# Optimization experiments

Measured on AMD Instinct MI355X. Metric: run time of the kernel, lower is better.

The kernel has to match this reference:

```python
import jax, jax.numpy as jnp
import numpy as np

V = 50000   # words_num
D = 128     # embedding_dim
B = 2048    # batch
P = 20      # max Huffman path length


def setup_inputs() -> dict:
    key = jax.random.key(0)
    k1, k2, k3, k4, k5 = jax.random.split(key, 5)
    inputs_vector = jax.random.uniform(k1, (B, V), dtype=jnp.float32)
    path_nodes_indices = jax.random.randint(k2, (B, P), 0, V)
    huffman_codes = jax.random.randint(k3, (B, P), 0, 2).astype(jnp.float32)
    mask = jnp.ones((B, P), dtype=jnp.float32)
    # learned params, torch nn.Linear weight layout [out, in], kaiming-uniform-ish scale
    W_emb = jax.random.uniform(k4, (D, V), dtype=jnp.float32, minval=-1.0, maxval=1.0) / np.sqrt(V)
    W_cls = jax.random.uniform(k5, (V, D), dtype=jnp.float32, minval=-1.0, maxval=1.0) / np.sqrt(D)
    return {
        "inputs_vector": inputs_vector,
        "W_emb": W_emb,
        "W_cls": W_cls,
        "path_nodes_indices": path_nodes_indices,
        "huffman_codes": huffman_codes,
        "mask": mask,
    }


def _bce_with_logits(logits, targets):
    # numerically stable, elementwise (reduction='none')
    return jnp.maximum(logits, 0.0) - logits * targets + jnp.log1p(jnp.exp(-jnp.abs(logits)))


def reference(inputs_vector, W_emb, W_cls, path_nodes_indices, huffman_codes, mask):
    x = inputs_vector @ W_emb.T              # [B, D]  embedding Linear (no bias)
    logits_full = x @ W_cls.T                # [B, V]  full-vocab cls matmul (as in source)
    logits = jnp.take_along_axis(logits_full, path_nodes_indices, axis=1)  # [B, P]
    loss = _bce_with_logits(logits, huffman_codes)  # [B, P]
    masked_loss = loss * mask
    per_sample = masked_loss.sum(axis=-1) / mask.sum(axis=-1)  # [B]
    return per_sample.mean()
```

## Files before the change

kernel.cpp:

```cpp
#include <hip/hip_runtime.h>
#include <hip/hip_bf16.h>

#define V 50000
#define D 128
#define B 2048
#define P 20

#define BM 128
#define NSPLIT 32
#define KC 1568
#define VPAD (NSPLIT * KC)
#define NSLICE (VPAD / 32)
#define NMT (B / BM)

typedef float  f32x4  __attribute__((ext_vector_type(4)));
typedef short  bf16x8 __attribute__((ext_vector_type(8)));
typedef unsigned int uint4v __attribute__((ext_vector_type(4)));

__device__ __forceinline__ unsigned int pk2(float a, float b) {
    return (__float_as_uint(b) & 0xFFFF0000u) | (__float_as_uint(a) >> 16);
}
__device__ __forceinline__ unsigned short f2bf(float f) {
    unsigned int u = __float_as_uint(f);
    return (unsigned short)((u + 0x7FFFu + ((u >> 16) & 1u)) >> 16);
}
__device__ __forceinline__ bf16x8 pack8(f32x4 lo, f32x4 hi) {
    union { uint4v u; bf16x8 h; } r;
    r.u.x = pk2(lo[0], lo[1]); r.u.y = pk2(lo[2], lo[3]);
    r.u.z = pk2(hi[0], hi[1]); r.u.w = pk2(hi[2], hi[3]);
    return r.h;
}
__device__ __forceinline__ void gload_lds16(const void* g, void* l) {
    __builtin_amdgcn_global_load_lds(
        (const __attribute__((address_space(1))) unsigned int*)g,
        (__attribute__((address_space(3))) unsigned int*)l, 16, 0, 0);
}

__global__ __launch_bounds__(256)
void w2v_wcast(const float* __restrict__ Wemb, unsigned short* __restrict__ WTF) {
    __shared__ unsigned short L[128 * 128];
    const int bk = blockIdx.x;
    const int t  = threadIdx.x;
    const int d = t >> 1, h = t & 1;
    const float* src = Wemb + (size_t)d * V + bk * 128 + h * 64;
#pragma unroll
    for (int j = 0; j < 8; ++j) {
        const int kg = bk * 128 + h * 64 + j * 8;
        f32x4 v0 = {0,0,0,0}, v1 = {0,0,0,0};
        if (kg + 8 <= V) {
            const f32x4* p = reinterpret_cast<const f32x4*>(src + j * 8);
            v0 = p[0]; v1 = p[1];
        }
        uint4v u;
        u.x = pk2(v0[0], v0[1]); u.y = pk2(v0[2], v0[3]);
        u.z = pk2(v1[0], v1[1]); u.w = pk2(v1[2], v1[3]);
        const int c8 = h * 8 + j;
        *reinterpret_cast<uint4v*>((char*)L + d * 256 + ((c8 ^ (d & 15)) << 4)) = u;
    }
    __syncthreads();
    const int w = t >> 6, l = t & 63;
    const int kg4 = l >> 4, fr = l & 15;
#pragma unroll
    for (int sl = 0; sl < 4; ++sl)
#pragma unroll
        for (int j2 = 0; j2 < 2; ++j2) {
            const int n  = w + j2 * 4;
            const int dd = n * 16 + fr;
            const int c8 = sl * 4 + kg4;
            uint4v u = *reinterpret_cast<const uint4v*>(
                (char*)L + dd * 256 + ((c8 ^ (dd & 15)) << 4));
            *reinterpret_cast<uint4v*>(
                (char*)WTF + ((size_t)(bk * 4 + sl) * 8 + n) * 1024 + l * 16) = u;
        }
}

template<int FAST>
__global__ __launch_bounds__(256, 2)
void w2v_gemm(const float* __restrict__ Ain, const void* __restrict__ Wsrc,
              void* __restrict__ part) {
    __shared__ char smem[65536];
    char* Wlds = smem + 32768;

    const int i   = blockIdx.x;
    const int xcd = i & 7;
    const int q   = i >> 3;
    const int s   = xcd * 4 + (q >> 4);
    const int mt  = q & 15;
    const int m0  = mt * BM;
    const int k0  = s * KC;
    const int kend = (k0 + KC < V) ? (k0 + KC) : V;
    const int nst  = (kend - k0 + 63) >> 6;

    const int tid  = threadIdx.x;
    const int lane = tid & 63;
    const int wid  = tid >> 6;
    const int w32  = wid * 32;
    const int fr   = lane & 15;
    const int kg4  = lane >> 4;

    f32x4 acc[2][8] = {};

    const int arow = tid >> 1;
    const int ah   = tid & 1;
    const float* aSrc = Ain + (size_t)(m0 + arow) * V + ah * 32;
    const unsigned short* WT = (const unsigned short*)Wsrc;
    const float*          Wf = (const float*)Wsrc;

    f32x4 aR[8];
    auto loadA = [&](int ks) {
#pragma unroll
        for (int j = 0; j < 8; ++j) {
            const bool ok = (ks + ah * 32 + j * 4 + 4 <= kend);
            const f32x4* p = reinterpret_cast<const f32x4*>(ok ? (aSrc + ks + j * 4)
                                                               : (aSrc + k0));
            f32x4 v = *p;
            if (!ok) v = f32x4{0.f, 0.f, 0.f, 0.f};
            aR[j] = v;
        }
    };
    auto writeA = [&](int buf) {
        char* base = smem + buf * 16384 + arow * 128;
#pragma unroll
        for (int j2 = 0; j2 < 4; ++j2) {
            uint4v u;
            u.x = pk2(aR[j2*2][0], aR[j2*2][1]);   u.y = pk2(aR[j2*2][2], aR[j2*2][3]);
            u.z = pk2(aR[j2*2+1][0], aR[j2*2+1][1]); u.w = pk2(aR[j2*2+1][2], aR[j2*2+1][3]);
            const int c8 = ah * 4 + j2;
            *reinterpret_cast<uint4v*>(base + ((c8 ^ (arow & 7)) << 4)) = u;
        }
    };
    auto stageW = [&](int buf, int ks5) {
#pragma unroll
        for (int j = 0; j < 4; ++j) {
            const int g = wid * 4 + j;
            const unsigned short* gp = WT + (size_t)(ks5 + (g >> 3)) * 4096
                                          + (g & 7) * 512 + lane * 8;
            gload_lds16(gp, Wlds + buf * 16384 + g * 1024);
        }
    };
    auto computeMicro = [&](int buf, int u) {
        bf16x8 af[2];
#pragma unroll
        for (int m = 0; m < 2; ++m) {
            const int r  = w32 + m * 16 + fr;
            const int c8 = u * 4 + kg4;
            af[m] = *reinterpret_cast<const bf16x8*>(
                smem + buf * 16384 + r * 128 + ((c8 ^ (r & 7)) << 4));
        }
#pragma unroll
        for (int n = 0; n < 8; ++n) {
            const bf16x8 wf = *reinterpret_cast<const bf16x8*>(
                Wlds + buf * 16384 + (u * 8 + n) * 1024 + lane * 16);
            acc[0][n] = __builtin_amdgcn_mfma_f32_16x16x32_bf16(af[0], wf, acc[0][n], 0, 0, 0);
            acc[1][n] = __builtin_amdgcn_mfma_f32_16x16x32_bf16(af[1], wf, acc[1][n], 0, 0, 0);
        }
    };

    if (FAST) {
        loadA(k0);
        stageW(0, s * 49);
        for (int t = 0; t < nst; ++t) {
            writeA(t & 1);
            const bool more = (t + 1 < nst);
            if (more) {
                loadA(k0 + (t + 1) * 64);
                stageW((t + 1) & 1, s * 49 + (t + 1) * 2);
                asm volatile("s_waitcnt vmcnt(12) lgkmcnt(0)" ::: "memory");
            } else {
                asm volatile("s_waitcnt vmcnt(0) lgkmcnt(0)" ::: "memory");
            }
            __builtin_amdgcn_s_barrier();
            computeMicro(t & 1, 0);
            computeMicro(t & 1, 1);
        }
    } else {
        bf16x8 wfr[8];
        for (int t = 0; t < nst; ++t) {
            const int ks = k0 + t * 64;
            loadA(ks);
            writeA(0);
            __syncthreads();
#pragma unroll
            for (int u = 0; u < 2; ++u) {
#pragma unroll
                for (int n = 0; n < 8; ++n) {
                    const int kg = ks + u * 32 + kg4 * 8;
                    f32x4 lo = {0,0,0,0}, hi = {0,0,0,0};
                    if (kg + 8 <= V) {
                        const f32x4* p = reinterpret_cast<const f32x4*>(
                            Wf + (size_t)(n * 16 + fr) * V + kg);
                        lo = p[0]; hi = p[1];
                    }
                    wfr[n] = pack8(lo, hi);
                }
                bf16x8 af[2];
#pragma unroll
                for (int m = 0; m < 2; ++m) {
                    const int r  = w32 + m * 16 + fr;
                    const int c8 = u * 4 + kg4;
                    af[m] = *reinterpret_cast<const bf16x8*>(
                        smem + r * 128 + ((c8 ^ (r & 7)) << 4));
                }
#pragma unroll
                for (int n = 0; n < 8; ++n) {
                    acc[0][n] = __builtin_amdgcn_mfma_f32_16x16x32_bf16(af[0], wfr[n], acc[0][n], 0, 0, 0);
                    acc[1][n] = __builtin_amdgcn_mfma_f32_16x16x32_bf16(af[1], wfr[n], acc[1][n], 0, 0, 0);
                }
            }
            __syncthreads();
        }
    }

    if (!FAST) {
        float* outp = (float*)part;
#pragma unroll
        for (int m = 0; m < 2; ++m) {
            const int r0 = m0 + w32 + m * 16 + kg4 * 4;
#pragma unroll
            for (int n = 0; n < 8; ++n) {
                const int c = n * 16 + fr;
#pragma unroll
                for (int jj = 0; jj < 4; ++jj)
                    atomicAdd(&outp[(size_t)(r0 + jj) * D + c], acc[m][n][jj]);
            }
        }
        return;
    }
    asm volatile("s_waitcnt lgkmcnt(0)" ::: "memory");
    __builtin_amdgcn_s_barrier();
    unsigned short* Cs = (unsigned short*)smem;
#pragma unroll
    for (int m = 0; m < 2; ++m) {
        const int r0 = w32 + m * 16 + kg4 * 4;
#pragma unroll
        for (int n = 0; n < 8; ++n) {
            const int c = n * 16 + fr;
#pragma unroll
            for (int jj = 0; jj < 4; ++jj)
                Cs[(r0 + jj) * 128 + c] = f2bf(acc[m][n][jj]);
        }
    }
    __syncthreads();
    char* dstb = (char*)part + ((size_t)s * B + m0) * (D * 2);
#pragma unroll
    for (int it = 0; it < 8; ++it) {
        const int off = (it * 256 + tid) * 16;
        uint4v v = *reinterpret_cast<const uint4v*>((char*)smem + off);
        *reinterpret_cast<uint4v*>(dstb + off) = v;
    }
}

__global__ __launch_bounds__(256)
void w2v_loss(const void* __restrict__ part, int part_bf16,
              const float* __restrict__ Wcls, const int* __restrict__ pathIdx,
              const float* __restrict__ codes, const float* __restrict__ mask,
              float* __restrict__ out) {
    const int lane = threadIdx.x & 63;
    const int wid  = threadIdx.x >> 6;
    const int b    = blockIdx.x * 4 + wid;

    float x0 = 0.f, x1 = 0.f;
    if (part_bf16) {
        const unsigned* pb = (const unsigned*)part;
#pragma unroll 8
        for (int s = 0; s < NSPLIT; ++s) {
            unsigned u = pb[((size_t)s * B + b) * 64 + lane];
            x0 += __uint_as_float(u << 16);
            x1 += __uint_as_float(u & 0xFFFF0000u);
        }
    } else {
        const float* pf = (const float*)part;
        const float2 v = *reinterpret_cast<const float2*>(&pf[(size_t)b * D + lane * 2]);
        x0 = v.x; x1 = v.y;
    }

    float lsum = 0.f, msum = 0.f;
#pragma unroll
    for (int p = 0; p < P; ++p) {
        int node = pathIdx[b * P + p];
        const float2 w = *reinterpret_cast<const float2*>(&Wcls[(size_t)node * D + lane * 2]);
        float d = x0 * w.x + x1 * w.y;
#pragma unroll
        for (int off = 1; off < 64; off <<= 1)
            d += __shfl_xor(d, off, 64);
        float t  = codes[b * P + p];
        float mm = mask[b * P + p];
        float loss = fmaxf(d, 0.f) - d * t + log1pf(__expf(-fabsf(d)));
        lsum += loss * mm;
        msum += mm;
    }
    float per = (msum > 0.f) ? (lsum / msum) : 0.f;

    __shared__ float wsum[4];
    if (lane == 0) wsum[wid] = per;
    __syncthreads();
    if (threadIdx.x == 0) {
        float ssum = wsum[0] + wsum[1] + wsum[2] + wsum[3];
        atomicAdd(out, ssum * (1.0f / (float)B));
    }
}

extern "C" void kernel_launch(void* const* d_in, const int* in_sizes, int n_in,
                              void* d_out, int out_size, void* d_ws, size_t ws_size,
                              hipStream_t stream) {
    const float* inputs = (const float*)d_in[0];
    const float* W_emb  = (const float*)d_in[1];
    const float* W_cls  = (const float*)d_in[2];
    const int*   path   = (const int*)  d_in[3];
    const float* codes  = (const float*)d_in[4];
    const float* mask   = (const float*)d_in[5];
    float* out = (float*)d_out;

    hipMemsetAsync(d_out, 0, sizeof(float), stream);

    const size_t wtf_bytes = (size_t)NSLICE * 8192;
    const size_t part_off  = (wtf_bytes + 255) & ~(size_t)255;
    const size_t part_need = part_off + (size_t)NSPLIT * B * D * 2;

    if (ws_size >= part_need) {
        unsigned short* WTF = (unsigned short*)d_ws;
        char* partp = (char*)d_ws + part_off;
        w2v_wcast<<<dim3(VPAD / 128), dim3(256), 0, stream>>>(W_emb, WTF);
        w2v_gemm<1><<<dim3(NMT * NSPLIT), dim3(256), 0, stream>>>(inputs, WTF, partp);
        w2v_loss<<<dim3(B / 4), dim3(256), 0, stream>>>(partp, 1, W_cls, path, codes, mask, out);
    } else {
        hipMemsetAsync(d_ws, 0, (size_t)B * D * sizeof(float), stream);
        w2v_gemm<0><<<dim3(NMT * NSPLIT), dim3(256), 0, stream>>>(inputs, W_emb, d_ws);
        w2v_loss<<<dim3(B / 4), dim3(256), 0, stream>>>(d_ws, 0, W_cls, path, codes, mask, out);
    }
}
```

Before: 170.6 us.

## Stage whole A K-chunk in LDS upfront and stream W from registers

Restructures the split-K GEMM: tiles shrink to 64 rows with 896-wide K chunks over 56 splits and 512-thread blocks. Each block loads its entire A slice into LDS once, converting to bf16 before a single barrier. W fragments are then read straight from global memory into double-buffered registers, replacing the per-step LDS staging and barriers. This is meant to remove per-iteration synchronisation and expose more parallelism, at the cost of larger LDS per block, more partial sums for the loss kernel to reduce, and no overlap between the A load and compute.

```diff
diff --git a/kernel.cpp b/kernel.cpp
--- a/kernel.cpp
+++ b/kernel.cpp
@@ -6,9 +6,10 @@
 #define B 2048
 #define P 20
 
-#define BM 128
-#define NSPLIT 32
-#define KC 1568
+#define BM 64
+#define KC 896
+#define NSTEP 14
+#define NSPLIT 56
 #define VPAD (NSPLIT * KC)
 #define NSLICE (VPAD / 32)
 #define NMT (B / BM)
@@ -16,6 +17,7 @@
 typedef float  f32x4  __attribute__((ext_vector_type(4)));
 typedef short  bf16x8 __attribute__((ext_vector_type(8)));
 typedef unsigned int uint4v __attribute__((ext_vector_type(4)));
+typedef unsigned int uint2v __attribute__((ext_vector_type(2)));
 
 __device__ __forceinline__ unsigned int pk2(float a, float b) {
     return (__float_as_uint(b) & 0xFFFF0000u) | (__float_as_uint(a) >> 16);
@@ -29,11 +31,6 @@
     r.u.x = pk2(lo[0], lo[1]); r.u.y = pk2(lo[2], lo[3]);
     r.u.z = pk2(hi[0], hi[1]); r.u.w = pk2(hi[2], hi[3]);
     return r.h;
-}
-__device__ __forceinline__ void gload_lds16(const void* g, void* l) {
-    __builtin_amdgcn_global_load_lds(
-        (const __attribute__((address_space(1))) unsigned int*)g,
-        (__attribute__((address_space(3))) unsigned int*)l, 16, 0, 0);
 }
 
 __global__ __launch_bounds__(256)
@@ -75,178 +72,125 @@
 }
 
 template<int FAST>
-__global__ __launch_bounds__(256, 2)
+__global__ __launch_bounds__(512, 2)
 void w2v_gemm(const float* __restrict__ Ain, const void* __restrict__ Wsrc,
               void* __restrict__ part) {
-    __shared__ char smem[65536];
-    char* Wlds = smem + 32768;
+    __shared__ char smem[NSTEP * 8192];
 
     const int i   = blockIdx.x;
     const int xcd = i & 7;
-    const int q   = i >> 3;
-    const int s   = xcd * 4 + (q >> 4);
-    const int mt  = q & 15;
+    const int j   = i >> 3;
+    const int s   = xcd * 7 + (j >> 5);
+    const int mt  = j & 31;
     const int m0  = mt * BM;
     const int k0  = s * KC;
     const int kend = (k0 + KC < V) ? (k0 + KC) : V;
-    const int nst  = (kend - k0 + 63) >> 6;
 
     const int tid  = threadIdx.x;
     const int lane = tid & 63;
     const int wid  = tid >> 6;
-    const int w32  = wid * 32;
+    const int rg   = wid & 3;
+    const int wc   = wid >> 2;
     const int fr   = lane & 15;
     const int kg4  = lane >> 4;
 
-    f32x4 acc[2][8] = {};
-
-    const int arow = tid >> 1;
-    const int ah   = tid & 1;
-    const float* aSrc = Ain + (size_t)(m0 + arow) * V + ah * 32;
+    {
+        const int row = tid >> 3;
+        const int q   = tid & 7;
+        const float* src = Ain + (size_t)(m0 + row) * V + k0 + q * 112;
+        char* wbase = smem + row * 128;
+#pragma unroll
+        for (int jj = 0; jj < 28; ++jj) {
+            const int f0 = q * 112 + jj * 4;
+            f32x4 v = {0.f, 0.f, 0.f, 0.f};
+            if (k0 + f0 + 4 <= kend)
+                v = *reinterpret_cast<const f32x4*>(src + jj * 4);
+            uint2v u; u.x = pk2(v[0], v[1]); u.y = pk2(v[2], v[3]);
+            const int tt = f0 >> 6, c8 = (f0 >> 3) & 7, hf = (f0 >> 2) & 1;
+            *reinterpret_cast<uint2v*>(wbase + tt * 8192 + ((c8 ^ (row & 7)) << 4) + hf * 8) = u;
+        }
+    }
+    __syncthreads();
+
+    f32x4 acc[4] = {};
     const unsigned short* WT = (const unsigned short*)Wsrc;
     const float*          Wf = (const float*)Wsrc;
 
-    f32x4 aR[8];
-    auto loadA = [&](int ks) {
-#pragma unroll
-        for (int j = 0; j < 8; ++j) {
-            const bool ok = (ks + ah * 32 + j * 4 + 4 <= kend);
-            const f32x4* p = reinterpret_cast<const f32x4*>(ok ? (aSrc + ks + j * 4)
-                                                               : (aSrc + k0));
-            f32x4 v = *p;
-            if (!ok) v = f32x4{0.f, 0.f, 0.f, 0.f};
-            aR[j] = v;
-        }
-    };
-    auto writeA = [&](int buf) {
-        char* base = smem + buf * 16384 + arow * 128;
-#pragma unroll
-        for (int j2 = 0; j2 < 4; ++j2) {
-            uint4v u;
-            u.x = pk2(aR[j2*2][0], aR[j2*2][1]);   u.y = pk2(aR[j2*2][2], aR[j2*2][3]);
-            u.z = pk2(aR[j2*2+1][0], aR[j2*2+1][1]); u.w = pk2(aR[j2*2+1][2], aR[j2*2+1][3]);
-            const int c8 = ah * 4 + j2;
-            *reinterpret_cast<uint4v*>(base + ((c8 ^ (arow & 7)) << 4)) = u;
-        }
-    };
-    auto stageW = [&](int buf, int ks5) {
-#pragma unroll
-        for (int j = 0; j < 4; ++j) {
-            const int g = wid * 4 + j;
-            const unsigned short* gp = WT + (size_t)(ks5 + (g >> 3)) * 4096
-                                          + (g & 7) * 512 + lane * 8;
-            gload_lds16(gp, Wlds + buf * 16384 + g * 1024);
-        }
-    };
-    auto computeMicro = [&](int buf, int u) {
-        bf16x8 af[2];
-#pragma unroll
-        for (int m = 0; m < 2; ++m) {
-            const int r  = w32 + m * 16 + fr;
-            const int c8 = u * 4 + kg4;
-            af[m] = *reinterpret_cast<const bf16x8*>(
-                smem + buf * 16384 + r * 128 + ((c8 ^ (r & 7)) << 4));
-        }
-#pragma unroll
-        for (int n = 0; n < 8; ++n) {
-            const bf16x8 wf = *reinterpret_cast<const bf16x8*>(
-                Wlds + buf * 16384 + (u * 8 + n) * 1024 + lane * 16);
-            acc[0][n] = __builtin_amdgcn_mfma_f32_16x16x32_bf16(af[0], wf, acc[0][n], 0, 0, 0);
-            acc[1][n] = __builtin_amdgcn_mfma_f32_16x16x32_bf16(af[1], wf, acc[1][n], 0, 0, 0);
-        }
-    };
-
-    if (FAST) {
-        loadA(k0);
-        stageW(0, s * 49);
-        for (int t = 0; t < nst; ++t) {
-            writeA(t & 1);
-            const bool more = (t + 1 < nst);
-            if (more) {
-                loadA(k0 + (t + 1) * 64);
-                stageW((t + 1) & 1, s * 49 + (t + 1) * 2);
-                asm volatile("s_waitcnt vmcnt(12) lgkmcnt(0)" ::: "memory");
-            } else {
-                asm volatile("s_waitcnt vmcnt(0) lgkmcnt(0)" ::: "memory");
-            }
-            __builtin_amdgcn_s_barrier();
-            computeMicro(t & 1, 0);
-            computeMicro(t & 1, 1);
-        }
-    } else {
-        bf16x8 wfr[8];
-        for (int t = 0; t < nst; ++t) {
-            const int ks = k0 + t * 64;
-            loadA(ks);
-            writeA(0);
-            __syncthreads();
-#pragma unroll
-            for (int u = 0; u < 2; ++u) {
-#pragma unroll
-                for (int n = 0; n < 8; ++n) {
-                    const int kg = ks + u * 32 + kg4 * 8;
+    bf16x8 wfA[8], wfB[8];
+    auto loadW = [&](bf16x8* wf, int t) {
+        if (FAST) {
+            const size_t ks5 = (size_t)s * 28 + t * 2;
+#pragma unroll
+            for (int u = 0; u < 2; ++u)
+#pragma unroll
+                for (int n = 0; n < 4; ++n)
+                    wf[u * 4 + n] = *reinterpret_cast<const bf16x8*>(
+                        (const char*)WT + (ks5 + u) * 8192 + (wc * 4 + n) * 1024 + lane * 16);
+        } else {
+#pragma unroll
+            for (int u = 0; u < 2; ++u)
+#pragma unroll
+                for (int n = 0; n < 4; ++n) {
+                    const int kg = k0 + t * 64 + u * 32 + kg4 * 8;
+                    const int dd = wc * 64 + n * 16 + fr;
                     f32x4 lo = {0,0,0,0}, hi = {0,0,0,0};
                     if (kg + 8 <= V) {
-                        const f32x4* p = reinterpret_cast<const f32x4*>(
-                            Wf + (size_t)(n * 16 + fr) * V + kg);
+                        const f32x4* p = reinterpret_cast<const f32x4*>(Wf + (size_t)dd * V + kg);
                         lo = p[0]; hi = p[1];
                     }
-                    wfr[n] = pack8(lo, hi);
+                    wf[u * 4 + n] = pack8(lo, hi);
                 }
-                bf16x8 af[2];
-#pragma unroll
-                for (int m = 0; m < 2; ++m) {
-                    const int r  = w32 + m * 16 + fr;
-                    const int c8 = u * 4 + kg4;
-                    af[m] = *reinterpret_cast<const bf16x8*>(
-                        smem + r * 128 + ((c8 ^ (r & 7)) << 4));
-                }
-#pragma unroll
-                for (int n = 0; n < 8; ++n) {
-                    acc[0][n] = __builtin_amdgcn_mfma_f32_16x16x32_bf16(af[0], wfr[n], acc[0][n], 0, 0, 0);
-                    acc[1][n] = __builtin_amdgcn_mfma_f32_16x16x32_bf16(af[1], wfr[n], acc[1][n], 0, 0, 0);
-                }
-            }
-            __syncthreads();
-        }
-    }
+        }
+    };
+    auto computeStep = [&](const bf16x8* wf, int t) {
+#pragma unroll
+        for (int u = 0; u < 2; ++u) {
+            const int r = rg * 16 + fr;
+            const bf16x8 af = *reinterpret_cast<const bf16x8*>(
+                smem + t * 8192 + r * 128 + (((u * 4 + kg4) ^ (r & 7)) << 4));
+#pragma unroll
+            for (int n = 0; n < 4; ++n)
+                acc[n] = __builtin_amdgcn_mfma_f32_16x16x32_bf16(af, wf[u * 4 + n], acc[n], 0, 0, 0);
+        }
+    };
+
+    loadW(wfA, 0);
+#pragma unroll
+    for (int t = 0; t < NSTEP; t += 2) {
+        loadW(wfB, t + 1);
+        computeStep(wfA, t);
+        if (t + 2 < NSTEP) loadW(wfA, t + 2);
+        computeStep(wfB, t + 1);
+    }
+
+    __syncthreads();
 
     if (!FAST) {
         float* outp = (float*)part;
 #pragma unroll
-        for (int m = 0; m < 2; ++m) {
-            const int r0 = m0 + w32 + m * 16 + kg4 * 4;
-#pragma unroll
-            for (int n = 0; n < 8; ++n) {
-                const int c = n * 16 + fr;
-#pragma unroll
-                for (int jj = 0; jj < 4; ++jj)
-                    atomicAdd(&outp[(size_t)(r0 + jj) * D + c], acc[m][n][jj]);
-            }
+        for (int n = 0; n < 4; ++n) {
+            const int c = wc * 64 + n * 16 + fr;
+#pragma unroll
+            for (int jj = 0; jj < 4; ++jj)
+                atomicAdd(&outp[(size_t)(m0 + rg * 16 + kg4 * 4 + jj) * D + c], acc[n][jj]);
         }
         return;
     }
-    asm volatile("s_waitcnt lgkmcnt(0)" ::: "memory");
-    __builtin_amdgcn_s_barrier();
     unsigned short* Cs = (unsigned short*)smem;
 #pragma unroll
-    for (int m = 0; m < 2; ++m) {
-        const int r0 = w32 + m * 16 + kg4 * 4;
-#pragma unroll
-        for (int n = 0; n < 8; ++n) {
-            const int c = n * 16 + fr;
-#pragma unroll
-            for (int jj = 0; jj < 4; ++jj)
-                Cs[(r0 + jj) * 128 + c] = f2bf(acc[m][n][jj]);
-        }
+    for (int n = 0; n < 4; ++n) {
+        const int c = wc * 64 + n * 16 + fr;
+#pragma unroll
+        for (int jj = 0; jj < 4; ++jj)
+            Cs[(rg * 16 + kg4 * 4 + jj) * 128 + c] = f2bf(acc[n][jj]);
     }
     __syncthreads();
     char* dstb = (char*)part + ((size_t)s * B + m0) * (D * 2);
 #pragma unroll
-    for (int it = 0; it < 8; ++it) {
-        const int off = (it * 256 + tid) * 16;
-        uint4v v = *reinterpret_cast<const uint4v*>((char*)smem + off);
-        *reinterpret_cast<uint4v*>(dstb + off) = v;
+    for (int it = 0; it < 2; ++it) {
+        const int off = (it * 512 + tid) * 16;
+        *reinterpret_cast<uint4v*>(dstb + off) =
+            *reinterpret_cast<const uint4v*>(smem + off);
     }
 }
 
@@ -321,11 +265,11 @@
         unsigned short* WTF = (unsigned short*)d_ws;
         char* partp = (char*)d_ws + part_off;
         w2v_wcast<<<dim3(VPAD / 128), dim3(256), 0, stream>>>(W_emb, WTF);
-        w2v_gemm<1><<<dim3(NMT * NSPLIT), dim3(256), 0, stream>>>(inputs, WTF, partp);
+        w2v_gemm<1><<<dim3(NMT * NSPLIT), dim3(512), 0, stream>>>(inputs, WTF, partp);
         w2v_loss<<<dim3(B / 4), dim3(256), 0, stream>>>(partp, 1, W_cls, path, codes, mask, out);
     } else {
         hipMemsetAsync(d_ws, 0, (size_t)B * D * sizeof(float), stream);
-        w2v_gemm<0><<<dim3(NMT * NSPLIT), dim3(256), 0, stream>>>(inputs, W_emb, d_ws);
+        w2v_gemm<0><<<dim3(NMT * NSPLIT), dim3(512), 0, stream>>>(inputs, W_emb, d_ws);
         w2v_loss<<<dim3(B / 4), dim3(256), 0, stream>>>(d_ws, 0, W_cls, path, codes, mask, out);
     }
 }
```

Result: slower. 248.1 us (+45.5%).

## Make A tiles wave-private in LDS, load W fragments directly to registers

Applied to the files above, without the earlier changes.

Each wave now stages only its own 32 rows of the A tile into a private LDS region laid out in MFMA fragment order. This removes the block-wide barrier from the K loop. W fragments are read straight from global memory into registers instead of through global_load_lds staging, which halves LDS use and allows 3 blocks per CU. The K split also goes from 32 to 48 chunks to fill more CUs. The trade-offs are that each wave re-reads W from global/L2 with less latency hiding, and there are more partial outputs to reduce. The epilogue also dropped its pre-barrier, which may be unsafe now that Cs overlays other waves' LDS regions.

```diff
diff --git a/kernel.cpp b/kernel.cpp
--- a/kernel.cpp
+++ b/kernel.cpp
@@ -7,8 +7,8 @@
 #define P 20
 
 #define BM 128
-#define NSPLIT 32
-#define KC 1568
+#define NSPLIT 48
+#define KC 1056
 #define VPAD (NSPLIT * KC)
 #define NSLICE (VPAD / 32)
 #define NMT (B / BM)
@@ -29,11 +29,6 @@
     r.u.x = pk2(lo[0], lo[1]); r.u.y = pk2(lo[2], lo[3]);
     r.u.z = pk2(hi[0], hi[1]); r.u.w = pk2(hi[2], hi[3]);
     return r.h;
-}
-__device__ __forceinline__ void gload_lds16(const void* g, void* l) {
-    __builtin_amdgcn_global_load_lds(
-        (const __attribute__((address_space(1))) unsigned int*)g,
-        (__attribute__((address_space(3))) unsigned int*)l, 16, 0, 0);
 }
 
 __global__ __launch_bounds__(256)
@@ -75,16 +70,15 @@
 }
 
 template<int FAST>
-__global__ __launch_bounds__(256, 2)
+__global__ __launch_bounds__(256, 3)
 void w2v_gemm(const float* __restrict__ Ain, const void* __restrict__ Wsrc,
               void* __restrict__ part) {
-    __shared__ char smem[65536];
-    char* Wlds = smem + 32768;
+    __shared__ char smem[32768];
 
     const int i   = blockIdx.x;
     const int xcd = i & 7;
     const int q   = i >> 3;
-    const int s   = xcd * 4 + (q >> 4);
+    const int s   = xcd * 6 + (q >> 4);
     const int mt  = q & 15;
     const int m0  = mt * BM;
     const int k0  = s * KC;
@@ -100,9 +94,12 @@
 
     f32x4 acc[2][8] = {};
 
-    const int arow = tid >> 1;
-    const int ah   = tid & 1;
+    const int arow = w32 + (lane >> 1);
+    const int ah   = lane & 1;
     const float* aSrc = Ain + (size_t)(m0 + arow) * V + ah * 32;
+    char* myLDS = smem + wid * 8192;
+    char* wBase = myLDS + ah * 2048 + (lane >> 5) * 1024 + ((lane >> 1) & 15) * 16;
+
     const unsigned short* WT = (const unsigned short*)Wsrc;
     const float*          Wf = (const float*)Wsrc;
 
@@ -110,105 +107,73 @@
     auto loadA = [&](int ks) {
 #pragma unroll
         for (int j = 0; j < 8; ++j) {
-            const bool ok = (ks + ah * 32 + j * 4 + 4 <= kend);
-            const f32x4* p = reinterpret_cast<const f32x4*>(ok ? (aSrc + ks + j * 4)
-                                                               : (aSrc + k0));
-            f32x4 v = *p;
-            if (!ok) v = f32x4{0.f, 0.f, 0.f, 0.f};
+            f32x4 v = {0.f, 0.f, 0.f, 0.f};
+            if (ks + ah * 32 + j * 4 + 4 <= kend)
+                v = *reinterpret_cast<const f32x4*>(aSrc + ks + j * 4);
             aR[j] = v;
         }
     };
     auto writeA = [&](int buf) {
-        char* base = smem + buf * 16384 + arow * 128;
+        char* base = wBase + buf * 4096;
 #pragma unroll
         for (int j2 = 0; j2 < 4; ++j2) {
             uint4v u;
-            u.x = pk2(aR[j2*2][0], aR[j2*2][1]);   u.y = pk2(aR[j2*2][2], aR[j2*2][3]);
-            u.z = pk2(aR[j2*2+1][0], aR[j2*2+1][1]); u.w = pk2(aR[j2*2+1][2], aR[j2*2+1][3]);
-            const int c8 = ah * 4 + j2;
-            *reinterpret_cast<uint4v*>(base + ((c8 ^ (arow & 7)) << 4)) = u;
+            u.x = pk2(aR[j2*2][0], aR[j2*2][1]);
+            u.y = pk2(aR[j2*2][2], aR[j2*2][3]);
+            u.z = pk2(aR[j2*2+1][0], aR[j2*2+1][1]);
+            u.w = pk2(aR[j2*2+1][2], aR[j2*2+1][3]);
+            *reinterpret_cast<uint4v*>(base + j2 * 256) = u;
         }
     };
-    auto stageW = [&](int buf, int ks5) {
-#pragma unroll
-        for (int j = 0; j < 4; ++j) {
-            const int g = wid * 4 + j;
-            const unsigned short* gp = WT + (size_t)(ks5 + (g >> 3)) * 4096
-                                          + (g & 7) * 512 + lane * 8;
-            gload_lds16(gp, Wlds + buf * 16384 + g * 1024);
+    bf16x8 wf[8];
+    auto loadWu = [&](int t, int u) {
+        if (FAST) {
+            const size_t ks5 = (size_t)(k0 + t * 64 + u * 32) >> 5;
+            const char* wb = (const char*)WT + ks5 * 8192 + lane * 16;
+#pragma unroll
+            for (int n = 0; n < 8; ++n)
+                wf[n] = *reinterpret_cast<const bf16x8*>(wb + n * 1024);
+        } else {
+            const int kg = k0 + t * 64 + u * 32 + kg4 * 8;
+#pragma unroll
+            for (int n = 0; n < 8; ++n) {
+                f32x4 lo = {0,0,0,0}, hi = {0,0,0,0};
+                if (kg + 8 <= V) {
+                    const f32x4* p = reinterpret_cast<const f32x4*>(
+                        Wf + (size_t)(n * 16 + fr) * V + kg);
+                    lo = p[0]; hi = p[1];
+                }
+                wf[n] = pack8(lo, hi);
+            }
         }
     };
-    auto computeMicro = [&](int buf, int u) {
-        bf16x8 af[2];
-#pragma unroll
-        for (int m = 0; m < 2; ++m) {
-            const int r  = w32 + m * 16 + fr;
-            const int c8 = u * 4 + kg4;
-            af[m] = *reinterpret_cast<const bf16x8*>(
-                smem + buf * 16384 + r * 128 + ((c8 ^ (r & 7)) << 4));
-        }
-#pragma unroll
-        for (int n = 0; n < 8; ++n) {
-            const bf16x8 wf = *reinterpret_cast<const bf16x8*>(
-                Wlds + buf * 16384 + (u * 8 + n) * 1024 + lane * 16);
-            acc[0][n] = __builtin_amdgcn_mfma_f32_16x16x32_bf16(af[0], wf, acc[0][n], 0, 0, 0);
-            acc[1][n] = __builtin_amdgcn_mfma_f32_16x16x32_bf16(af[1], wf, acc[1][n], 0, 0, 0);
-        }
-    };
-
-    if (FAST) {
-        loadA(k0);
-        stageW(0, s * 49);
-        for (int t = 0; t < nst; ++t) {
-            writeA(t & 1);
-            const bool more = (t + 1 < nst);
-            if (more) {
-                loadA(k0 + (t + 1) * 64);
-                stageW((t + 1) & 1, s * 49 + (t + 1) * 2);
-                asm volatile("s_waitcnt vmcnt(12) lgkmcnt(0)" ::: "memory");
-            } else {
-                asm volatile("s_waitcnt vmcnt(0) lgkmcnt(0)" ::: "memory");
-            }
-            __builtin_amdgcn_s_barrier();
-            computeMicro(t & 1, 0);
-            computeMicro(t & 1, 1);
-        }
-    } else {
-        bf16x8 wfr[8];
-        for (int t = 0; t < nst; ++t) {
-            const int ks = k0 + t * 64;
-            loadA(ks);
-            writeA(0);
-            __syncthreads();
-#pragma unroll
-            for (int u = 0; u < 2; ++u) {
-#pragma unroll
-                for (int n = 0; n < 8; ++n) {
-                    const int kg = ks + u * 32 + kg4 * 8;
-                    f32x4 lo = {0,0,0,0}, hi = {0,0,0,0};
-                    if (kg + 8 <= V) {
-                        const f32x4* p = reinterpret_cast<const f32x4*>(
-                            Wf + (size_t)(n * 16 + fr) * V + kg);
-                        lo = p[0]; hi = p[1];
-                    }
-                    wfr[n] = pack8(lo, hi);
-                }
-                bf16x8 af[2];
-#pragma unroll
-                for (int m = 0; m < 2; ++m) {
-                    const int r  = w32 + m * 16 + fr;
-                    const int c8 = u * 4 + kg4;
-                    af[m] = *reinterpret_cast<const bf16x8*>(
-                        smem + r * 128 + ((c8 ^ (r & 7)) << 4));
-                }
-#pragma unroll
-                for (int n = 0; n < 8; ++n) {
-                    acc[0][n] = __builtin_amdgcn_mfma_f32_16x16x32_bf16(af[0], wfr[n], acc[0][n], 0, 0, 0);
-                    acc[1][n] = __builtin_amdgcn_mfma_f32_16x16x32_bf16(af[1], wfr[n], acc[1][n], 0, 0, 0);
-                }
-            }
-            __syncthreads();
-        }
+
+    int cur = 0;
+    loadA(k0);
+    for (int t = 0; t < nst; ++t) {
+        writeA(cur);
+        loadWu(t, 0);
+        if (t + 1 < nst) loadA(k0 + (t + 1) * 64);
+        {
+            const bf16x8 af0 = *reinterpret_cast<const bf16x8*>(myLDS + cur*4096 + lane*16);
+            const bf16x8 af1 = *reinterpret_cast<const bf16x8*>(myLDS + cur*4096 + 1024 + lane*16);
+#pragma unroll
+            for (int n = 0; n < 8; ++n) {
+                acc[0][n] = __builtin_amdgcn_mfma_f32_16x16x32_bf16(af0, wf[n], acc[0][n], 0, 0, 0);
+                acc[1][n] = __builtin_amdgcn_mfma_f32_16x16x32_bf16(af1, wf[n], acc[1][n], 0, 0, 0);
+            }
+        }
+        loadWu(t, 1);
+        {
+            const bf16x8 af0 = *reinterpret_cast<const bf16x8*>(myLDS + cur*4096 + 2048 + lane*16);
+            const bf16x8 af1 = *reinterpret_cast<const bf16x8*>(myLDS + cur*4096 + 3072 + lane*16);
+#pragma unroll
+            for (int n = 0; n < 8; ++n) {
+                acc[0][n] = __builtin_amdgcn_mfma_f32_16x16x32_bf16(af0, wf[n], acc[0][n], 0, 0, 0);
+                acc[1][n] = __builtin_amdgcn_mfma_f32_16x16x32_bf16(af1, wf[n], acc[1][n], 0, 0, 0);
+            }
+        }
+        cur ^= 1;
     }
 
     if (!FAST) {
@@ -226,8 +191,6 @@
         }
         return;
     }
-    asm volatile("s_waitcnt lgkmcnt(0)" ::: "memory");
-    __builtin_amdgcn_s_barrier();
     unsigned short* Cs = (unsigned short*)smem;
 #pragma unroll
     for (int m = 0; m < 2; ++m) {
```

Result: slower. 204.4 us (+19.8%).
